# Performance work log

Measured on AMD Instinct MI355X. Metric: run time of the kernel, lower is better.

Reference implementation:

```python
import jax, jax.numpy as jnp
import numpy as np

N = 524288
D_IN = 14
HID = 128
LAT = 5
VOCAB = 256
BETA = 0.25


def setup_inputs() -> dict:
    key = jax.random.key(0)
    ks = jax.random.split(key, 12)
    s = lambda fi: 1.0 / np.sqrt(fi)
    inp = {
        "x": jax.random.normal(ks[0], (N, D_IN), jnp.float32),
        "enc_w1": jax.random.uniform(ks[1], (D_IN, HID), jnp.float32, -s(D_IN), s(D_IN)),
        "enc_b1": jnp.zeros((HID,), jnp.float32),
        "enc_w2": jax.random.uniform(ks[2], (HID, HID), jnp.float32, -s(HID), s(HID)),
        "enc_b2": jnp.zeros((HID,), jnp.float32),
        "enc_w3": jax.random.uniform(ks[3], (HID, LAT), jnp.float32, -s(HID), s(HID)),
        "enc_b3": jnp.zeros((LAT,), jnp.float32),
        "emb": jax.random.uniform(ks[4], (VOCAB, LAT), jnp.float32, -1.0 / VOCAB, 1.0 / VOCAB),
        "dec_w1": jax.random.uniform(ks[5], (LAT, HID), jnp.float32, -s(LAT), s(LAT)),
        "dec_b1": jnp.zeros((HID,), jnp.float32),
        "dec_w2": jax.random.uniform(ks[6], (HID, D_IN), jnp.float32, -s(HID), s(HID)),
        "dec_b2": jnp.zeros((D_IN,), jnp.float32),
    }
    return inp


def reference(x, enc_w1, enc_b1, enc_w2, enc_b2, enc_w3, enc_b3, emb,
              dec_w1, dec_b1, dec_w2, dec_b2):
    # encoder MLP: [N,14] -> [N,5]
    h = jax.nn.relu(x @ enc_w1 + enc_b1)
    h = jax.nn.relu(h @ enc_w2 + enc_b2)
    quant_input = h @ enc_w3 + enc_b3  # [N, LAT]

    # squared distances to codebook (argmin identical to cdist argmin)
    d2 = (jnp.sum(quant_input * quant_input, axis=1, keepdims=True)
          - 2.0 * quant_input @ emb.T
          + jnp.sum(emb * emb, axis=1)[None, :])  # [N, VOCAB]
    min_idx = jnp.argmin(d2, axis=1)                       # [N]
    min_encoding_indices = min_idx[:, None]                # [N, 1]
    min_encodings = jax.nn.one_hot(min_idx, VOCAB, dtype=quant_input.dtype)  # [N, VOCAB]

    # gather via one-hot matmul, as in the original
    quant_out = min_encodings @ emb                        # [N, LAT]

    e_mean = jnp.mean(min_encodings, axis=0)
    perplexity = jnp.exp(-jnp.sum(e_mean * jnp.log(e_mean + 1e-10)))

    sg = jax.lax.stop_gradient
    code_book_loss = jnp.mean((sg(quant_input) - quant_out) ** 2)
    commitment_loss = jnp.mean((quant_input - sg(quant_out)) ** 2)
    quant_loss = code_book_loss + BETA * commitment_loss

    # straight-through estimator
    quant_out = quant_input + sg(quant_out - quant_input)

    # decoder MLP: [N,5] -> [N,14]
    h = jax.nn.relu(quant_out @ dec_w1 + dec_b1)
    output = h @ dec_w2 + dec_b2
    return output, quant_loss, perplexity, min_encodings, min_encoding_indices
```

## Files before the change

### kernel.cpp

```cpp
#include <hip/hip_runtime.h>
#include <cstdint>
#include <cstddef>

#define NROWS 524288
#define DIN 14
#define HID 128
#define LAT 5
#define VOCAB 256
#define BR 64
#define NT 512
#define HS 132

#define FENCE(v) asm volatile("" : "+v"(v))

static constexpr size_t LOSS_OFF = 7340032;
static constexpr size_t PERP_OFF = 7340033;
static constexpr size_t OH_OFF   = 7340034;
static constexpr size_t IDX_OFF  = 141557762;

static constexpr int OFF_WBUF = 0;
static constexpr int OFF_EMB8 = 0;
static constexpr int OFF_W3T  = 2048;
static constexpr int OFF_DW1T = 2712;
static constexpr int OFF_DW2T = 3736;
static constexpr int OFF_B3   = 5584;
static constexpr int OFF_DB1  = 5592;
static constexpr int OFF_DB2  = 5720;
static constexpr int OFF_Q    = 5736;
static constexpr int OFF_QE4  = 6056;
static constexpr int OFF_QE1  = 6312;
static constexpr int OFF_IDX  = 6376;
static constexpr int OFF_HIST = 6440;
static constexpr int OFF_RED  = 6696;
static constexpr int OFF_H    = 8192;
static constexpr int OFF_W1T  = 16640;
static constexpr int OFF_B1   = 19200;
static constexpr int OFF_B2   = 19328;
static constexpr int SMEM_FLOATS = 19456;
static constexpr int SMEM_BYTES  = SMEM_FLOATS * 4;
static_assert(SMEM_BYTES <= 80*1024, "need <=80KB for 2 blocks/CU");
static_assert((OFF_W3T%4)==0 && (OFF_DW1T%4)==0 && (OFF_DW2T%4)==0 &&
              (OFF_QE4%4)==0 && (OFF_H%4)==0 && (OFF_W1T%4)==0, "align");

__global__ __launch_bounds__(NT, 4)
void vqvae_main(const float* __restrict__ x,
                const float* __restrict__ ew1, const float* __restrict__ eb1,
                const float* __restrict__ ew2, const float* __restrict__ eb2,
                const float* __restrict__ ew3, const float* __restrict__ eb3,
                const float* __restrict__ emb,
                const float* __restrict__ dw1, const float* __restrict__ db1,
                const float* __restrict__ dw2, const float* __restrict__ db2,
                float* __restrict__ out,
                double* __restrict__ loss_sum,
                unsigned int* __restrict__ hist_g)
{
    #pragma clang fp contract(off)

    extern __shared__ float smem[];
    float* s_wbuf = smem + OFF_WBUF;
    float* s_h    = smem + OFF_H;
    float* s_w1t  = smem + OFF_W1T;
    float* s_b1   = smem + OFF_B1;
    float* s_b2   = smem + OFF_B2;
    float* s_emb8 = smem + OFF_EMB8;
    float* s_w3t  = smem + OFF_W3T;
    float* s_dw1t = smem + OFF_DW1T;
    float* s_dw2t = smem + OFF_DW2T;
    float* s_b3   = smem + OFF_B3;
    float* s_db1  = smem + OFF_DB1;
    float* s_db2  = smem + OFF_DB2;
    float* s_q    = smem + OFF_Q;
    float* s_qe4  = smem + OFF_QE4;
    float* s_qe1  = smem + OFF_QE1;
    int*   s_idx  = reinterpret_cast<int*>(smem + OFF_IDX);
    unsigned int* s_hist = reinterpret_cast<unsigned int*>(smem + OFF_HIST);
    float* s_red  = smem + OFF_RED;

    const int tid = threadIdx.x;
    const int r_base = blockIdx.x * BR;

    {
        float4* wb4 = reinterpret_cast<float4*>(s_wbuf);
        const float4* w2g = reinterpret_cast<const float4*>(ew2);
        for (int i = tid; i < 2048; i += NT) wb4[i] = w2g[i];
        for (int i = tid; i < DIN*HID; i += NT) {
            const int k = i >> 7, c = i & 127;
            s_w1t[c*20 + k] = ew1[i];
        }
        if (tid < HID) { s_b1[tid] = eb1[tid]; s_b2[tid] = eb2[tid]; }
    }
    __syncthreads();

    {
        const int r  = tid >> 3;
        const int q8 = tid & 7;
        const float* xrow = x + (size_t)(r_base + r) * DIN;
        float xr[DIN];
        #pragma unroll
        for (int k = 0; k < DIN; k += 2) {
            float2 v = *reinterpret_cast<const float2*>(xrow + k);
            xr[k] = v.x; xr[k+1] = v.y;
        }
        for (int cc = 0; cc < HID/8; ++cc) {
            const int c = q8 + 8*cc;
            const float4 wq0 = *reinterpret_cast<const float4*>(&s_w1t[c*20 + 0]);
            const float4 wq1 = *reinterpret_cast<const float4*>(&s_w1t[c*20 + 4]);
            const float4 wq2 = *reinterpret_cast<const float4*>(&s_w1t[c*20 + 8]);
            const float4 wq3 = *reinterpret_cast<const float4*>(&s_w1t[c*20 + 12]);
            const float w[14] = {wq0.x,wq0.y,wq0.z,wq0.w, wq1.x,wq1.y,wq1.z,wq1.w,
                                 wq2.x,wq2.y,wq2.z,wq2.w, wq3.x,wq3.y};
            float s = 0.f;
            #pragma unroll
            for (int k = 0; k < DIN; ++k) { s = fmaf(xr[k], w[k], s); FENCE(s); }
            s = s + s_b1[c]; FENCE(s);
            s_h[r*HS + c] = fmaxf(s, 0.f);
        }
    }
    __syncthreads();

    {
        const int trow = tid >> 4;
        const int tcol = tid & 15;
        const int r0 = trow * 2, c0 = tcol * 8;
        float accE[2][8], accO[2][8];
        #pragma unroll
        for (int i = 0; i < 2; ++i)
            #pragma unroll
            for (int j = 0; j < 8; ++j) { accE[i][j] = 0.f; accO[i][j] = 0.f; }

        #pragma unroll 1
        for (int pass = 0; pass < 2; ++pass) {
            const int kbase = pass * 64;
            for (int kk = 0; kk < 64; kk += 2) {
                float hvE[2], hvO[2];
                #pragma unroll
                for (int i = 0; i < 2; ++i) {
                    const float2 hp = *reinterpret_cast<const float2*>(&s_h[(r0+i)*HS + kbase + kk]);
                    hvE[i] = hp.x; hvO[i] = hp.y;
                }
                float4 waE = *reinterpret_cast<const float4*>(&s_wbuf[kk*HID + c0]);
                float4 wbE = *reinterpret_cast<const float4*>(&s_wbuf[kk*HID + c0 + 4]);
                float4 waO = *reinterpret_cast<const float4*>(&s_wbuf[(kk+1)*HID + c0]);
                float4 wbO = *reinterpret_cast<const float4*>(&s_wbuf[(kk+1)*HID + c0 + 4]);
                float wE[8] = {waE.x, waE.y, waE.z, waE.w, wbE.x, wbE.y, wbE.z, wbE.w};
                float wO[8] = {waO.x, waO.y, waO.z, waO.w, wbO.x, wbO.y, wbO.z, wbO.w};
                #pragma unroll
                for (int i = 0; i < 2; ++i)
                    #pragma unroll
                    for (int j = 0; j < 8; ++j) {
                        accE[i][j] = fmaf(hvE[i], wE[j], accE[i][j]); FENCE(accE[i][j]);
                        accO[i][j] = fmaf(hvO[i], wO[j], accO[i][j]); FENCE(accO[i][j]);
                    }
            }
            __syncthreads();
            if (pass == 0) {
                float4* wb4 = reinterpret_cast<float4*>(s_wbuf);
                const float4* w2g = reinterpret_cast<const float4*>(ew2);
                for (int i = tid; i < 2048; i += NT) wb4[i] = w2g[i + 2048];
                __syncthreads();
            }
        }
        #pragma unroll
        for (int i = 0; i < 2; ++i)
            #pragma unroll
            for (int j = 0; j < 8; ++j) {
                const int c = c0 + j;
                float s = accE[i][j] + accO[i][j]; FENCE(s);
                s = s + s_b2[c]; FENCE(s);
                s_h[(r0+i)*HS + c] = fmaxf(s, 0.f);
            }
    }
    __syncthreads();

    {
        for (int i = tid; i < VOCAB*LAT; i += NT) {
            const int v = i / 5, k = i - 5*v;
            s_emb8[v*8 + k] = emb[i];
        }
        for (int i = tid; i < HID*LAT; i += NT) {
            const int k = i / 5, c = i - 5*k;
            s_w3t[c*132 + k] = ew3[i];
        }
        for (int i = tid; i < LAT*HID; i += NT) {
            const int k = i >> 7, c = i & 127;
            s_dw1t[c*8 + k] = dw1[i];
        }
        for (int i = tid; i < HID*DIN; i += NT) {
            const int k = i / 14, c = i - 14*k;
            s_dw2t[c*132 + k] = dw2[i];
        }
        if (tid < LAT) s_b3[tid] = eb3[tid];
        if (tid < HID) s_db1[tid] = db1[tid];
        if (tid < DIN) s_db2[tid] = db2[tid];
        if (tid < VOCAB) s_hist[tid] = 0u;
    }
    __syncthreads();

    if (tid < VOCAB) {
        const float* e8 = &s_emb8[tid*8];
        float p0 = e8[0]*e8[0];
        float p1 = e8[1]*e8[1];
        float p2 = e8[2]*e8[2];
        float p3 = e8[3]*e8[3];
        float p4 = e8[4]*e8[4];
        float e = p0 + p1; FENCE(e);
        e = e + p2; FENCE(e);
        e = e + p3; FENCE(e);
        e = e + p4; FENCE(e);
        s_emb8[tid*8 + 5] = e;
    }
    if (tid < BR*LAT) {
        const int r = tid / LAT;
        const int c = tid - r*LAT;
        float s = 0.f;
        for (int kq = 0; kq < HID; kq += 4) {
            const float4 hq = *reinterpret_cast<const float4*>(&s_h[r*HS + kq]);
            const float4 wq = *reinterpret_cast<const float4*>(&s_w3t[c*132 + kq]);
            s = fmaf(hq.x, wq.x, s); FENCE(s);
            s = fmaf(hq.y, wq.y, s); FENCE(s);
            s = fmaf(hq.z, wq.z, s); FENCE(s);
            s = fmaf(hq.w, wq.w, s); FENCE(s);
        }
        s = s + s_b3[c]; FENCE(s);
        s_q[r*LAT + c] = s;
    }
    __syncthreads();

    float loss_local = 0.f;
    {
        const int r  = tid >> 3;
        const int q8 = tid & 7;
        float qv[LAT];
        #pragma unroll
        for (int k = 0; k < LAT; ++k) qv[k] = s_q[r*LAT + k];

        float qp0 = qv[0]*qv[0];
        float qp1 = qv[1]*qv[1];
        float qp2 = qv[2]*qv[2];
        float qp3 = qv[3]*qv[3];
        float qp4 = qv[4]*qv[4];
        float qq = qp0 + qp1; FENCE(qq);
        qq = qq + qp2; FENCE(qq);
        qq = qq + qp3; FENCE(qq);
        qq = qq + qp4; FENCE(qq);

        float bd = 3.4e38f; int bv = VOCAB;
        for (int ii = 0; ii < VOCAB/8; ++ii) {
            const int v = q8 + 8*ii;
            const float4 elo = *reinterpret_cast<const float4*>(&s_emb8[v*8]);
            const float4 ehi = *reinterpret_cast<const float4*>(&s_emb8[v*8 + 4]);
            float dot = 0.f;
            dot = fmaf(qv[4], ehi.x, dot); FENCE(dot);
            dot = fmaf(qv[3], elo.w, dot); FENCE(dot);
            dot = fmaf(qv[2], elo.z, dot); FENCE(dot);
            dot = fmaf(qv[1], elo.y, dot); FENCE(dot);
            dot = fmaf(qv[0], elo.x, dot); FENCE(dot);
            float twodot = 2.0f * dot; FENCE(twodot);
            float t1 = qq - twodot; FENCE(t1);
            float sc = t1 + ehi.y; FENCE(sc);
            const bool better = (sc < bd) || (sc == bd && v < bv);
            bd = better ? sc : bd;
            bv = better ? v  : bv;
        }
        #pragma unroll
        for (int m = 1; m <= 4; m <<= 1) {
            const float od = __shfl_xor(bd, m);
            const int   ov = __shfl_xor(bv, m);
            const bool better = (od < bd) || (od == bd && ov < bv);
            bd = better ? od : bd;
            bv = better ? ov : bv;
        }
        if (q8 == 0) {
            s_idx[r] = bv;
            atomicAdd(&s_hist[bv], 1u);
            float ls = 0.f;
            #pragma unroll
            for (int k = 0; k < LAT; ++k) {
                const float d = qv[k] - s_emb8[bv*8 + k];
                ls = fmaf(d, d, ls);
            }
            loss_local = ls;
            #pragma unroll
            for (int k = 0; k < 4; ++k) {
                const float ev = s_emb8[bv*8 + k];
                s_qe4[r*4 + k] = qv[k] + (ev - qv[k]);
            }
            {
                const float ev = s_emb8[bv*8 + 4];
                s_qe1[r] = qv[4] + (ev - qv[4]);
            }
        }
    }

    {
        float s = loss_local;
        #pragma unroll
        for (int off = 32; off > 0; off >>= 1) s += __shfl_down(s, off);
        if ((tid & 63) == 0) s_red[tid >> 6] = s;
    }
    __syncthreads();
    if (tid == 0) {
        float s = 0.f;
        #pragma unroll
        for (int w = 0; w < NT/64; ++w) s += s_red[w];
        atomicAdd(loss_sum, (double)s);
    }
    if (tid < VOCAB) {
        const unsigned c = s_hist[tid];
        if (c) atomicAdd(&hist_g[tid], c);
    }

    {
        float* oh = out + OH_OFF;
        const int rr0 = tid >> 7;
        const int c0  = (tid & 127) * 2;
        for (int it = 0; it < BR/4; ++it) {
            const int r = it*4 + rr0;
            const int best = s_idx[r];
            float2 v;
            v.x = (c0     == best) ? 1.f : 0.f;
            v.y = (c0 + 1 == best) ? 1.f : 0.f;
            *reinterpret_cast<float2*>(oh + (size_t)(r_base + r)*VOCAB + c0) = v;
        }
        if (tid < BR) out[IDX_OFF + r_base + tid] = (float)s_idx[tid];
    }

    {
        const int r  = tid >> 3;
        const int q8 = tid & 7;
        const float4 qlo = *reinterpret_cast<const float4*>(&s_qe4[r*4]);
        const float qe4v = s_qe1[r];
        for (int cc = 0; cc < HID/8; ++cc) {
            const int c = q8 + 8*cc;
            const float4 wq = *reinterpret_cast<const float4*>(&s_dw1t[c*8]);
            const float w4 = s_dw1t[c*8 + 4];
            float s = 0.f;
            s = fmaf(qlo.x, wq.x, s);
            s = fmaf(qlo.y, wq.y, s);
            s = fmaf(qlo.z, wq.z, s);
            s = fmaf(qlo.w, wq.w, s);
            s = fmaf(qe4v,  w4,   s);
            s_h[r*HS + c] = fmaxf(s + s_db1[c], 0.f);
        }
    }
    __syncthreads();

    for (int oi = tid; oi < BR*DIN; oi += NT) {
        const int r = oi / DIN;
        const int c = oi - r*DIN;
        float s = 0.f;
        for (int kq = 0; kq < HID; kq += 4) {
            const float4 hq = *reinterpret_cast<const float4*>(&s_h[r*HS + kq]);
            const float4 wq = *reinterpret_cast<const float4*>(&s_dw2t[c*132 + kq]);
            s = fmaf(hq.x, wq.x, s);
            s = fmaf(hq.y, wq.y, s);
            s = fmaf(hq.z, wq.z, s);
            s = fmaf(hq.w, wq.w, s);
        }
        out[(size_t)r_base*DIN + oi] = s + s_db2[c];
    }
}

__global__ void vq_init(double* loss, unsigned int* hist)
{
    if (threadIdx.x == 0) *loss = 0.0;
    if (threadIdx.x < VOCAB) hist[threadIdx.x] = 0u;
}

__global__ void vq_final(const double* __restrict__ loss,
                         const unsigned int* __restrict__ hist,
                         float* __restrict__ out)
{
    #pragma clang fp contract(off)
    __shared__ float red[4];
    const int t = threadIdx.x;
    const float em = (float)hist[t] / (float)NROWS;
    float s = em * logf(em + 1e-10f);
    #pragma unroll
    for (int off = 32; off > 0; off >>= 1) s += __shfl_down(s, off);
    if ((t & 63) == 0) red[t >> 6] = s;
    __syncthreads();
    if (t == 0) {
        const float tot = red[0] + red[1] + red[2] + red[3];
        out[PERP_OFF] = expf(-tot);
        out[LOSS_OFF] = 1.25f * (float)(*loss / (double)((size_t)NROWS * LAT));
    }
}

extern "C" void kernel_launch(void* const* d_in, const int* in_sizes, int n_in,
                              void* d_out, int out_size, void* d_ws, size_t ws_size,
                              hipStream_t stream)
{
    const float* x   = (const float*)d_in[0];
    const float* ew1 = (const float*)d_in[1];
    const float* eb1 = (const float*)d_in[2];
    const float* ew2 = (const float*)d_in[3];
    const float* eb2 = (const float*)d_in[4];
    const float* ew3 = (const float*)d_in[5];
    const float* eb3 = (const float*)d_in[6];
    const float* emb = (const float*)d_in[7];
    const float* dw1 = (const float*)d_in[8];
    const float* db1 = (const float*)d_in[9];
    const float* dw2 = (const float*)d_in[10];
    const float* db2 = (const float*)d_in[11];
    float* out = (float*)d_out;

    double* loss = (double*)d_ws;
    unsigned int* hist = (unsigned int*)((char*)d_ws + 8);

    hipFuncSetAttribute(reinterpret_cast<const void*>(vqvae_main),
                        hipFuncAttributeMaxDynamicSharedMemorySize, SMEM_BYTES);

    vq_init<<<1, 256, 0, stream>>>(loss, hist);
    vqvae_main<<<NROWS / BR, NT, SMEM_BYTES, stream>>>(
        x, ew1, eb1, ew2, eb2, ew3, eb3, emb, dw1, db1, dw2, db2,
        out, loss, hist);
    vq_final<<<1, 256, 0, stream>>>(loss, hist, out);
}
```

Measured before the change: 1.072 ms.

## Warp-specialize GEMM2: half the threads compute, half zero-fill one-hot output

```diff
diff --git a/kernel.cpp b/kernel.cpp
--- a/kernel.cpp
+++ b/kernel.cpp
@@ -121,56 +121,115 @@
     {
         const int trow = tid >> 4;
         const int tcol = tid & 15;
-        const int r0 = trow * 2, c0 = tcol * 8;
-        float accE[2][8], accO[2][8];
-        #pragma unroll
-        for (int i = 0; i < 2; ++i)
+        const int r0 = trow * 4, c0 = tcol * 8;
+        float accE[4][8], accO[4][8];
+        #pragma unroll
+        for (int i = 0; i < 4; ++i)
             #pragma unroll
             for (int j = 0; j < 8; ++j) { accE[i][j] = 0.f; accO[i][j] = 0.f; }
 
-        #pragma unroll 1
-        for (int pass = 0; pass < 2; ++pass) {
-            const int kbase = pass * 64;
-            for (int kk = 0; kk < 64; kk += 2) {
-                float hvE[2], hvO[2];
+        if (tid < 256) {
+            for (int kk = 0; kk < 64; kk += 4) {
+                float4 h4[4];
                 #pragma unroll
-                for (int i = 0; i < 2; ++i) {
-                    const float2 hp = *reinterpret_cast<const float2*>(&s_h[(r0+i)*HS + kbase + kk]);
-                    hvE[i] = hp.x; hvO[i] = hp.y;
+                for (int i = 0; i < 4; ++i)
+                    h4[i] = *reinterpret_cast<const float4*>(&s_h[(r0+i)*HS + kk]);
+                {
+                    float4 waE = *reinterpret_cast<const float4*>(&s_wbuf[kk*HID + c0]);
+                    float4 wbE = *reinterpret_cast<const float4*>(&s_wbuf[kk*HID + c0 + 4]);
+                    float4 waO = *reinterpret_cast<const float4*>(&s_wbuf[(kk+1)*HID + c0]);
+                    float4 wbO = *reinterpret_cast<const float4*>(&s_wbuf[(kk+1)*HID + c0 + 4]);
+                    float wE[8] = {waE.x,waE.y,waE.z,waE.w, wbE.x,wbE.y,wbE.z,wbE.w};
+                    float wO[8] = {waO.x,waO.y,waO.z,waO.w, wbO.x,wbO.y,wbO.z,wbO.w};
+                    #pragma unroll
+                    for (int i = 0; i < 4; ++i)
+                        #pragma unroll
+                        for (int j = 0; j < 8; ++j) {
+                            accE[i][j] = fmaf(h4[i].x, wE[j], accE[i][j]); FENCE(accE[i][j]);
+                            accO[i][j] = fmaf(h4[i].y, wO[j], accO[i][j]); FENCE(accO[i][j]);
+                        }
                 }
-                float4 waE = *reinterpret_cast<const float4*>(&s_wbuf[kk*HID + c0]);
-                float4 wbE = *reinterpret_cast<const float4*>(&s_wbuf[kk*HID + c0 + 4]);
-                float4 waO = *reinterpret_cast<const float4*>(&s_wbuf[(kk+1)*HID + c0]);
-                float4 wbO = *reinterpret_cast<const float4*>(&s_wbuf[(kk+1)*HID + c0 + 4]);
-                float wE[8] = {waE.x, waE.y, waE.z, waE.w, wbE.x, wbE.y, wbE.z, wbE.w};
-                float wO[8] = {waO.x, waO.y, waO.z, waO.w, wbO.x, wbO.y, wbO.z, wbO.w};
+                {
+                    float4 waE = *reinterpret_cast<const float4*>(&s_wbuf[(kk+2)*HID + c0]);
+                    float4 wbE = *reinterpret_cast<const float4*>(&s_wbuf[(kk+2)*HID + c0 + 4]);
+                    float4 waO = *reinterpret_cast<const float4*>(&s_wbuf[(kk+3)*HID + c0]);
+                    float4 wbO = *reinterpret_cast<const float4*>(&s_wbuf[(kk+3)*HID + c0 + 4]);
+                    float wE[8] = {waE.x,waE.y,waE.z,waE.w, wbE.x,wbE.y,wbE.z,wbE.w};
+                    float wO[8] = {waO.x,waO.y,waO.z,waO.w, wbO.x,wbO.y,wbO.z,wbO.w};
+                    #pragma unroll
+                    for (int i = 0; i < 4; ++i)
+                        #pragma unroll
+                        for (int j = 0; j < 8; ++j) {
+                            accE[i][j] = fmaf(h4[i].z, wE[j], accE[i][j]); FENCE(accE[i][j]);
+                            accO[i][j] = fmaf(h4[i].w, wO[j], accO[i][j]); FENCE(accO[i][j]);
+                        }
+                }
+            }
+        } else {
+            float4* oh4 = reinterpret_cast<float4*>(out + OH_OFF + (size_t)r_base*VOCAB);
+            const float4 z = {0.f, 0.f, 0.f, 0.f};
+            const int t = tid - 256;
+            #pragma unroll
+            for (int it = 0; it < 16; ++it) oh4[it*256 + t] = z;
+        }
+        __syncthreads();
+        {
+            float4* wb4 = reinterpret_cast<float4*>(s_wbuf);
+            const float4* w2g = reinterpret_cast<const float4*>(ew2);
+            for (int i = tid; i < 2048; i += NT) wb4[i] = w2g[i + 2048];
+        }
+        __syncthreads();
+        if (tid < 256) {
+            for (int kk = 0; kk < 64; kk += 4) {
+                float4 h4[4];
                 #pragma unroll
-                for (int i = 0; i < 2; ++i)
+                for (int i = 0; i < 4; ++i)
+                    h4[i] = *reinterpret_cast<const float4*>(&s_h[(r0+i)*HS + 64 + kk]);
+                {
+                    float4 waE = *reinterpret_cast<const float4*>(&s_wbuf[kk*HID + c0]);
+                    float4 wbE = *reinterpret_cast<const float4*>(&s_wbuf[kk*HID + c0 + 4]);
+                    float4 waO = *reinterpret_cast<const float4*>(&s_wbuf[(kk+1)*HID + c0]);
+                    float4 wbO = *reinterpret_cast<const float4*>(&s_wbuf[(kk+1)*HID + c0 + 4]);
+                    float wE[8] = {waE.x,waE.y,waE.z,waE.w, wbE.x,wbE.y,wbE.z,wbE.w};
+                    float wO[8] = {waO.x,waO.y,waO.z,waO.w, wbO.x,wbO.y,wbO.z,wbO.w};
                     #pragma unroll
-                    for (int j = 0; j < 8; ++j) {
-                        accE[i][j] = fmaf(hvE[i], wE[j], accE[i][j]); FENCE(accE[i][j]);
-                        accO[i][j] = fmaf(hvO[i], wO[j], accO[i][j]); FENCE(accO[i][j]);
-                    }
+                    for (int i = 0; i < 4; ++i)
+                        #pragma unroll
+                        for (int j = 0; j < 8; ++j) {
+                            accE[i][j] = fmaf(h4[i].x, wE[j], accE[i][j]); FENCE(accE[i][j]);
+                            accO[i][j] = fmaf(h4[i].y, wO[j], accO[i][j]); FENCE(accO[i][j]);
+                        }
+                }
+                {
+                    float4 waE = *reinterpret_cast<const float4*>(&s_wbuf[(kk+2)*HID + c0]);
+                    float4 wbE = *reinterpret_cast<const float4*>(&s_wbuf[(kk+2)*HID + c0 + 4]);
+                    float4 waO = *reinterpret_cast<const float4*>(&s_wbuf[(kk+3)*HID + c0]);
+                    float4 wbO = *reinterpret_cast<const float4*>(&s_wbuf[(kk+3)*HID + c0 + 4]);
+                    float wE[8] = {waE.x,waE.y,waE.z,waE.w, wbE.x,wbE.y,wbE.z,wbE.w};
+                    float wO[8] = {waO.x,waO.y,waO.z,waO.w, wbO.x,wbO.y,wbO.z,wbO.w};
+                    #pragma unroll
+                    for (int i = 0; i < 4; ++i)
+                        #pragma unroll
+                        for (int j = 0; j < 8; ++j) {
+                            accE[i][j] = fmaf(h4[i].z, wE[j], accE[i][j]); FENCE(accE[i][j]);
+                            accO[i][j] = fmaf(h4[i].w, wO[j], accO[i][j]); FENCE(accO[i][j]);
+                        }
+                }
             }
-            __syncthreads();
-            if (pass == 0) {
-                float4* wb4 = reinterpret_cast<float4*>(s_wbuf);
-                const float4* w2g = reinterpret_cast<const float4*>(ew2);
-                for (int i = tid; i < 2048; i += NT) wb4[i] = w2g[i + 2048];
-                __syncthreads();
-            }
-        }
-        #pragma unroll
-        for (int i = 0; i < 2; ++i)
-            #pragma unroll
-            for (int j = 0; j < 8; ++j) {
-                const int c = c0 + j;
-                float s = accE[i][j] + accO[i][j]; FENCE(s);
-                s = s + s_b2[c]; FENCE(s);
-                s_h[(r0+i)*HS + c] = fmaxf(s, 0.f);
-            }
-    }
-    __syncthreads();
+        }
+        __syncthreads();
+        if (tid < 256) {
+            #pragma unroll
+            for (int i = 0; i < 4; ++i)
+                #pragma unroll
+                for (int j = 0; j < 8; ++j) {
+                    const int c = c0 + j;
+                    float s = accE[i][j] + accO[i][j]; FENCE(s);
+                    s = s + s_b2[c]; FENCE(s);
+                    s_h[(r0+i)*HS + c] = fmaxf(s, 0.f);
+                }
+        }
+    }
 
     {
         for (int i = tid; i < VOCAB*LAT; i += NT) {
@@ -265,7 +324,7 @@
         #pragma unroll
         for (int m = 1; m <= 4; m <<= 1) {
             const float od = __shfl_xor(bd, m);
-            const int   ov = __shfl_xor(bv, m);
+            const int    ov = __shfl_xor(bv, m);
             const bool better = (od < bd) || (od == bd && ov < bv);
             bd = better ? od : bd;
             bv = better ? ov : bv;
@@ -280,6 +339,8 @@
                 ls = fmaf(d, d, ls);
             }
             loss_local = ls;
+            out[OH_OFF + (size_t)(r_base + r)*VOCAB + bv] = 1.0f;
+            out[IDX_OFF + r_base + r] = (float)bv;
             #pragma unroll
             for (int k = 0; k < 4; ++k) {
                 const float ev = s_emb8[bv*8 + k];
@@ -308,21 +369,6 @@
     if (tid < VOCAB) {
         const unsigned c = s_hist[tid];
         if (c) atomicAdd(&hist_g[tid], c);
-    }
-
-    {
-        float* oh = out + OH_OFF;
-        const int rr0 = tid >> 7;
-        const int c0  = (tid & 127) * 2;
-        for (int it = 0; it < BR/4; ++it) {
-            const int r = it*4 + rr0;
-            const int best = s_idx[r];
-            float2 v;
-            v.x = (c0     == best) ? 1.f : 0.f;
-            v.y = (c0 + 1 == best) ? 1.f : 0.f;
-            *reinterpret_cast<float2*>(oh + (size_t)(r_base + r)*VOCAB + c0) = v;
-        }
-        if (tid < BR) out[IDX_OFF + r_base + tid] = (float)s_idx[tid];
     }
 
     {
```

Measured after the change: 1.027 ms. 4.2% less time.
